# Performance work log

Hardware: AMD Instinct MI355X
Metric: run time of the kernel (lower is better)

The kernel has to match this reference:

```python
import jax, jax.numpy as jnp
import numpy as np
from jax import lax

SEQ_LEN = 1024
INPUT_DIM = 64
NUM_HIDDEN = 512
NUM_CLASSES = 10
BATCH = 256
SIGMA = 0.01


def setup_inputs() -> dict:
    key = jax.random.key(0)
    k_x, k_whx, k_whh, k_wph = jax.random.split(key, 4)
    x = jax.random.normal(k_x, (BATCH, SEQ_LEN, INPUT_DIM), dtype=jnp.float32)
    Whx = SIGMA * jax.random.normal(k_whx, (INPUT_DIM, NUM_HIDDEN), dtype=jnp.float32)
    Whh = SIGMA * jax.random.normal(k_whh, (NUM_HIDDEN, NUM_HIDDEN), dtype=jnp.float32)
    Wph = SIGMA * jax.random.normal(k_wph, (NUM_HIDDEN, NUM_CLASSES), dtype=jnp.float32)
    bh = jnp.zeros((NUM_HIDDEN, 1), dtype=jnp.float32)
    bp = jnp.zeros((NUM_CLASSES, 1), dtype=jnp.float32)
    return {"x": x, "Whx": Whx, "Whh": Whh, "Wph": Wph, "bh": bh, "bp": bp}


def reference(x, Whx, Whh, Wph, bh, bp):
    # x: [B, S, D]; h: [B, H]
    B = x.shape[0]
    H = Whh.shape[0]
    bh_row = bh[:, 0]  # per-hidden-unit bias (intended semantics of bh)
    bp_row = bp[:, 0]

    def step(h, xt):
        h_new = jnp.tanh(xt @ Whx + h @ Whh + bh_row)
        return h_new, None

    h0 = jnp.zeros((B, H), dtype=x.dtype)
    xs = jnp.swapaxes(x, 0, 1)  # [S, B, D] for scan over time
    h_final, _ = lax.scan(step, h0, xs)
    p = h_final @ Wph + bp_row  # [B, C]
    return p
```

## Files before the change

### kernel.cpp

```cpp
#include <hip/hip_runtime.h>
#include <hip/hip_bf16.h>
#include <hip/hip_fp8.h>
#include <cstdint>
#include <cstddef>


#define T_SEQ   1024
#define D_IN    64
#define H_DIM   512
#define NB      16
#define NBLK    16
#define NTW     4
#define KS_F16  10
#define KS_REG8 2
#define KS_LDS8 4
#define HSPLIT  320
#define APITCH  848
#define FP8OFF  640
#define ABUF_BYTES (2 * NB * APITCH)
#define WWAVE_BYTES (KS_LDS8 * 2 * 1024)
#define WLDS_BYTES (8 * WWAVE_BYTES)
#define SMEM_TOTAL (ABUF_BYTES + WLDS_BYTES)
#define WSCALE  256.0f
#define HSCALE  128.0f
#define UNSCALE (1.0f / 32768.0f)
#define U_BYTES ((size_t)256 * 1024 * 512 * 2)
#define TT      16

typedef __attribute__((ext_vector_type(8))) short  short8;
typedef __attribute__((ext_vector_type(4))) short  short4v;
typedef __attribute__((ext_vector_type(4))) float  f32x4;
typedef __attribute__((ext_vector_type(2))) _Float16 h2v;
typedef __attribute__((ext_vector_type(4))) unsigned int uint4v;
typedef __attribute__((ext_vector_type(2))) unsigned int uint2v;

static __device__ __forceinline__ short f16b(float v) {
  return __builtin_bit_cast(short, (_Float16)v);
}
static __device__ __forceinline__ short bf16b(float v) {
  return __builtin_bit_cast(short, __float2bfloat16(v));
}
static __device__ __forceinline__ float f16f(unsigned short u) {
  return (float)__builtin_bit_cast(_Float16, (short)u);
}
static __device__ __forceinline__ unsigned int pk2h(float a, float b) {
#if defined(__has_builtin) && __has_builtin(__builtin_amdgcn_cvt_pkrtz)
  return __builtin_bit_cast(unsigned int, __builtin_amdgcn_cvt_pkrtz(a, b));
#else
  return (unsigned int)(unsigned short)f16b(a) |
         ((unsigned int)(unsigned short)f16b(b) << 16);
#endif
}
static __device__ __forceinline__ float fast_tanh(float x) {
  x = fminf(20.f, fmaxf(-20.f, x));
  const float t = __builtin_amdgcn_exp2f(x * 2.885390081777927f);
  return (t - 1.f) * __builtin_amdgcn_rcpf(t + 1.f);
}
static __device__ __forceinline__ unsigned char f32_to_fp8(float v) {
#if defined(__has_builtin) && __has_builtin(__builtin_amdgcn_cvt_pk_fp8_f32)
  const int r = __builtin_amdgcn_cvt_pk_fp8_f32(v, v, 0, false);
  return (unsigned char)(r & 0xff);
#else
  __hip_fp8_e4m3 f(v);
  return (unsigned char)f.__x;
#endif
}
static __device__ __forceinline__ unsigned int pk4fp8(float a, float b, float c, float d) {
#if defined(__has_builtin) && __has_builtin(__builtin_amdgcn_cvt_pk_fp8_f32)
  int r = __builtin_amdgcn_cvt_pk_fp8_f32(a, b, 0, false);
  r = __builtin_amdgcn_cvt_pk_fp8_f32(c, d, r, true);
  return (unsigned int)r;
#else
  return (unsigned int)f32_to_fp8(a) | ((unsigned int)f32_to_fp8(b) << 8) |
         ((unsigned int)f32_to_fp8(c) << 16) | ((unsigned int)f32_to_fp8(d) << 24);
#endif
}
static __device__ __forceinline__ float fp8_to_f32(unsigned char b) {
  __hip_fp8_e4m3 f;
  f.__x = (__hip_fp8_storage_t)b;
  return (float)f;
}

__global__ __launch_bounds__(512, 2)
void rnn_u_precompute(const float* __restrict__ x, const float* __restrict__ Whx,
                      const float* __restrict__ bh, char* __restrict__ U)
{
  const int tid  = threadIdx.x;
  const int lane = tid & 63;
  const int w    = tid >> 6;
  const int n16  = lane & 15;
  const int kq   = lane >> 4;
  const int rbase = blockIdx.x * NB;
  const int cwave = w * 64;

  short8 wa[2][NTW];
  #pragma unroll
  for (int s = 0; s < 2; ++s) {
    #pragma unroll
    for (int nt = 0; nt < NTW; ++nt) {
      const int c = cwave + nt * 16 + n16;
      short8 f;
      #pragma unroll
      for (int j = 0; j < 8; ++j)
        f[j] = f16b(Whx[(size_t)(s * 32 + kq * 8 + j) * H_DIM + c]);
      wa[s][nt] = f;
    }
  }
  f32x4 bb[NTW];
  #pragma unroll
  for (int nt = 0; nt < NTW; ++nt) {
    #pragma unroll
    for (int i = 0; i < 4; ++i) bb[nt][i] = bh[cwave + nt * 16 + kq * 4 + i];
  }

  const int b = rbase + n16;
  for (int tt = 0; tt < TT; ++tt) {
    const int t = blockIdx.y * TT + tt;
    short8 xb[2];
    #pragma unroll
    for (int s = 0; s < 2; ++s) {
      const float* px = x + ((size_t)b * T_SEQ + t) * D_IN + s * 32 + kq * 8;
      const f32x4 v0 = *(const f32x4*)px;
      const f32x4 v1 = *(const f32x4*)(px + 4);
      short8 f;
      f[0]=f16b(v0.x); f[1]=f16b(v0.y); f[2]=f16b(v0.z); f[3]=f16b(v0.w);
      f[4]=f16b(v1.x); f[5]=f16b(v1.y); f[6]=f16b(v1.z); f[7]=f16b(v1.w);
      xb[s] = f;
    }
    f32x4 D[NTW];
    #pragma unroll
    for (int nt = 0; nt < NTW; ++nt) {
      D[nt] = bb[nt];
      D[nt] = __builtin_amdgcn_mfma_f32_16x16x32_f16(wa[0][nt], xb[0], D[nt], 0, 0, 0);
      D[nt] = __builtin_amdgcn_mfma_f32_16x16x32_f16(wa[1][nt], xb[1], D[nt], 0, 0, 0);
    }
    uint4v o0, o1;
    o0.x = pk2h(D[0][0], D[0][1]); o0.y = pk2h(D[0][2], D[0][3]);
    o0.z = pk2h(D[1][0], D[1][1]); o0.w = pk2h(D[1][2], D[1][3]);
    o1.x = pk2h(D[2][0], D[2][1]); o1.y = pk2h(D[2][2], D[2][3]);
    o1.z = pk2h(D[3][0], D[3][1]); o1.w = pk2h(D[3][2], D[3][3]);
    char* dst = U + (((size_t)t * NBLK + blockIdx.x) * 512 + tid) * 32;
    *(uint4v*)dst = o0;
    *(uint4v*)(dst + 16) = o1;
  }
}

__global__ __launch_bounds__(512, 2)
void VanillaRNN_70025146794452_kernel(
    const float* __restrict__ Whh,
    const float* __restrict__ Wph,
    const float* __restrict__ bp,
    const char* __restrict__ U,
    float* __restrict__ out)
{
  const int tid  = threadIdx.x;
  const int lane = tid & 63;
  const int w    = tid >> 6;
  const int n16  = lane & 15;
  const int kq   = lane >> 4;
  const int rbase = blockIdx.x * NB;
  const int cwave = w * 64;

  extern __shared__ char smem[];
  char* Ab  = smem;
  char* Wlw = smem + ABUF_BYTES + w * WWAVE_BYTES;

  short8 wr[KS_F16][NTW];
  #pragma unroll
  for (int s = 0; s < KS_F16; ++s) {
    #pragma unroll
    for (int nt = 0; nt < NTW; ++nt) {
      const int c = cwave + nt * 16 + n16;
      short8 f;
      #pragma unroll
      for (int j = 0; j < 8; ++j)
        f[j] = f16b(Whh[(size_t)(s * 32 + kq * 8 + j) * H_DIM + c]);
      wr[s][nt] = f;
    }
  }
  long long wf8[KS_REG8][NTW];
  #pragma unroll
  for (int s = 0; s < KS_REG8; ++s) {
    #pragma unroll
    for (int nt = 0; nt < NTW; ++nt) {
      const int c  = cwave + nt * 16 + n16;
      const int k0 = (KS_F16 + s) * 32 + kq * 8;
      unsigned int lo = 0, hi = 0;
      #pragma unroll
      for (int bi = 0; bi < 4; ++bi) {
        lo |= ((unsigned int)f32_to_fp8(Whh[(size_t)(k0 + bi) * H_DIM + c] * WSCALE)) << (8 * bi);
        hi |= ((unsigned int)f32_to_fp8(Whh[(size_t)(k0 + 4 + bi) * H_DIM + c] * WSCALE)) << (8 * bi);
      }
      wf8[s][nt] = (long long)(((unsigned long long)hi << 32) | lo);
    }
  }
  for (int sl = 0; sl < KS_LDS8; ++sl) {
    for (int half = 0; half < 2; ++half) {
      const int k0 = (KS_F16 + KS_REG8 + sl) * 32 + kq * 8;
      unsigned int bqq[4];
      #pragma unroll
      for (int hh = 0; hh < 2; ++hh) {
        const int c = cwave + (2 * half + hh) * 16 + n16;
        #pragma unroll
        for (int u = 0; u < 2; ++u) {
          unsigned int acc = 0;
          #pragma unroll
          for (int bi = 0; bi < 4; ++bi)
            acc |= ((unsigned int)f32_to_fp8(Whh[(size_t)(k0 + u * 4 + bi) * H_DIM + c] * WSCALE)) << (8 * bi);
          bqq[hh * 2 + u] = acc;
        }
      }
      uint4v pk; pk.x = bqq[0]; pk.y = bqq[1]; pk.z = bqq[2]; pk.w = bqq[3];
      *(uint4v*)(Wlw + (size_t)(sl * 2 + half) * 1024 + lane * 16) = pk;
    }
  }

  for (int i = tid; i < ABUF_BYTES / 4; i += 512) ((int*)Ab)[i] = 0;
  uint4v Upf0, Upf1;
  {
    const char* up = U + (((size_t)0 * NBLK + blockIdx.x) * 512 + tid) * 32;
    Upf0 = *(const uint4v*)up;
    Upf1 = *(const uint4v*)(up + 16);
  }

  f32x4 C[NTW], C2[NTW];

  for (int t = 0; t < T_SEQ; ++t) {
    __syncthreads();
    char* Ac = Ab + (t & 1) * (NB * APITCH);
    char* An = Ab + ((t + 1) & 1) * (NB * APITCH);

    C[0][0]=f16f(Upf0.x&0xffff); C[0][1]=f16f(Upf0.x>>16);
    C[0][2]=f16f(Upf0.y&0xffff); C[0][3]=f16f(Upf0.y>>16);
    C[1][0]=f16f(Upf0.z&0xffff); C[1][1]=f16f(Upf0.z>>16);
    C[1][2]=f16f(Upf0.w&0xffff); C[1][3]=f16f(Upf0.w>>16);
    C[2][0]=f16f(Upf1.x&0xffff); C[2][1]=f16f(Upf1.x>>16);
    C[2][2]=f16f(Upf1.y&0xffff); C[2][3]=f16f(Upf1.y>>16);
    C[3][0]=f16f(Upf1.z&0xffff); C[3][1]=f16f(Upf1.z>>16);
    C[3][2]=f16f(Upf1.w&0xffff); C[3][3]=f16f(Upf1.w>>16);
    #pragma unroll
    for (int nt = 0; nt < NTW; ++nt) C2[nt] = (f32x4){0.f, 0.f, 0.f, 0.f};
    {
      const int t1 = (t + 1 < T_SEQ) ? (t + 1) : (T_SEQ - 1);
      const char* up = U + (((size_t)t1 * NBLK + blockIdx.x) * 512 + tid) * 32;
      Upf0 = *(const uint4v*)up;
      Upf1 = *(const uint4v*)(up + 16);
    }

    short8 hb = *(const short8*)(Ac + n16 * APITCH + 0 * 64 + kq * 16);
    #pragma unroll
    for (int s = 0; s < KS_F16; ++s) {
      const short8 a = hb;
      if (s + 1 < KS_F16)
        hb = *(const short8*)(Ac + n16 * APITCH + (s + 1) * 64 + kq * 16);
      #pragma unroll
      for (int nt = 0; nt < NTW; ++nt)
        C[nt] = __builtin_amdgcn_mfma_f32_16x16x32_f16(wr[s][nt], a, C[nt], 0, 0, 0);
    }
    #pragma unroll
    for (int s = 0; s < KS_REG8; ++s) {
      const long long h8 = *(const long long*)(Ac + n16 * APITCH + FP8OFF + s * 32 + kq * 8);
      #pragma unroll
      for (int nt = 0; nt < NTW; ++nt)
        C2[nt] = __builtin_amdgcn_mfma_f32_16x16x32_fp8_fp8(wf8[s][nt], h8, C2[nt], 0, 0, 0);
    }
    #pragma unroll
    for (int sl = 0; sl < KS_LDS8; ++sl) {
      const long long h8 = *(const long long*)(Ac + n16 * APITCH + FP8OFF + (KS_REG8 + sl) * 32 + kq * 8);
      const uint4v q0 = *(const uint4v*)(Wlw + (size_t)(sl * 2 + 0) * 1024 + lane * 16);
      const uint4v q1 = *(const uint4v*)(Wlw + (size_t)(sl * 2 + 1) * 1024 + lane * 16);
      const long long w0 = (long long)(((unsigned long long)q0.y << 32) | q0.x);
      const long long w1 = (long long)(((unsigned long long)q0.w << 32) | q0.z);
      const long long w2 = (long long)(((unsigned long long)q1.y << 32) | q1.x);
      const long long w3 = (long long)(((unsigned long long)q1.w << 32) | q1.z);
      C2[0] = __builtin_amdgcn_mfma_f32_16x16x32_fp8_fp8(w0, h8, C2[0], 0, 0, 0);
      C2[1] = __builtin_amdgcn_mfma_f32_16x16x32_fp8_fp8(w1, h8, C2[1], 0, 0, 0);
      C2[2] = __builtin_amdgcn_mfma_f32_16x16x32_fp8_fp8(w2, h8, C2[2], 0, 0, 0);
      C2[3] = __builtin_amdgcn_mfma_f32_16x16x32_fp8_fp8(w3, h8, C2[3], 0, 0, 0);
    }

    char* drow = An + n16 * APITCH;
    if (cwave < HSPLIT) {
      #pragma unroll
      for (int nt = 0; nt < NTW; ++nt) {
        const int c0 = cwave + nt * 16 + kq * 4;
        float v0 = fast_tanh(fmaf(C2[nt][0], UNSCALE, C[nt][0]));
        float v1 = fast_tanh(fmaf(C2[nt][1], UNSCALE, C[nt][1]));
        float v2 = fast_tanh(fmaf(C2[nt][2], UNSCALE, C[nt][2]));
        float v3 = fast_tanh(fmaf(C2[nt][3], UNSCALE, C[nt][3]));
        uint2v o; o.x = pk2h(v0, v1); o.y = pk2h(v2, v3);
        *(uint2v*)(drow + c0 * 2) = o;
      }
    } else {
      #pragma unroll
      for (int nt = 0; nt < NTW; ++nt) {
        const int c0 = cwave + nt * 16 + kq * 4;
        float v0 = fast_tanh(fmaf(C2[nt][0], UNSCALE, C[nt][0]));
        float v1 = fast_tanh(fmaf(C2[nt][1], UNSCALE, C[nt][1]));
        float v2 = fast_tanh(fmaf(C2[nt][2], UNSCALE, C[nt][2]));
        float v3 = fast_tanh(fmaf(C2[nt][3], UNSCALE, C[nt][3]));
        *(unsigned int*)(drow + FP8OFF + (c0 - HSPLIT)) =
            pk4fp8(v0 * HSCALE, v1 * HSCALE, v2 * HSCALE, v3 * HSCALE);
      }
    }
  }

  __syncthreads();
  if (tid < NB * 10) {
    const int r = tid / 10, c = tid % 10;
    const char* row = Ab + r * APITCH;
    float acc = bp[c];
    #pragma unroll 8
    for (int k = 0; k < HSPLIT; ++k)
      acc += f16f(*(const unsigned short*)(row + k * 2)) * Wph[k * 10 + c];
    #pragma unroll 8
    for (int k = HSPLIT; k < H_DIM; ++k)
      acc += fp8_to_f32((unsigned char)row[FP8OFF + (k - HSPLIT)]) * (1.f / HSCALE) * Wph[k * 10 + c];
    out[(size_t)(rbase + r) * 10 + c] = acc;
  }
}

#define FB_APITCH  1040
#define FB_FP8OFF  768
#define FB_ABUF    (2 * NB * FB_APITCH)
#define FB_WWAVE   (6 * 2 * 1024)
#define FB_SMEM    (FB_ABUF + 8 * FB_WWAVE)

__global__ __launch_bounds__(512, 2)
void rnn_fallback_kernel(
    const float* __restrict__ x, const float* __restrict__ Whx,
    const float* __restrict__ Whh, const float* __restrict__ Wph,
    const float* __restrict__ bh, const float* __restrict__ bp,
    float* __restrict__ out)
{
  const int tid = threadIdx.x, lane = tid & 63, w = tid >> 6;
  const int n16 = lane & 15, kq = lane >> 4;
  const int rbase = blockIdx.x * NB, cwave = w * 64;
  extern __shared__ char smem[];
  char* Ab  = smem;
  char* Wlw = smem + FB_ABUF + w * FB_WWAVE;

  short8 wr[12 * 4];
  #pragma unroll
  for (int s = 0; s < 12; ++s)
    #pragma unroll
    for (int nt = 0; nt < 4; ++nt) {
      const int c = cwave + nt * 16 + n16, k0 = s * 32 + kq * 8;
      short8 f;
      #pragma unroll
      for (int j = 0; j < 8; ++j) {
        const int k = k0 + j;
        const float* src = (k < D_IN) ? (Whx + (size_t)k * H_DIM + c)
                                      : (Whh + (size_t)(k - D_IN) * H_DIM + c);
        f[j] = bf16b(*src);
      }
      wr[s * 4 + nt] = f;
    }
  for (int s = 0; s < 6; ++s)
    for (int pp = 0; pp < 2; ++pp) {
      const int k0 = (12 + s) * 32 + kq * 8;
      unsigned int bq[4];
      #pragma unroll
      for (int half = 0; half < 2; ++half) {
        const int c = cwave + (2 * pp + half) * 16 + n16;
        #pragma unroll
        for (int u = 0; u < 2; ++u) {
          unsigned int acc = 0;
          #pragma unroll
          for (int bi = 0; bi < 4; ++bi)
            acc |= ((unsigned int)f32_to_fp8(Whh[(size_t)(k0 + u * 4 + bi - D_IN) * H_DIM + c] * WSCALE)) << (8 * bi);
          bq[half * 2 + u] = acc;
        }
      }
      uint4v pk; pk.x = bq[0]; pk.y = bq[1]; pk.z = bq[2]; pk.w = bq[3];
      *(uint4v*)(Wlw + (size_t)(s * 2 + pp) * 1024 + lane * 16) = pk;
    }
  float bhreg[4];
  #pragma unroll
  for (int nt = 0; nt < 4; ++nt) bhreg[nt] = bh[cwave + nt * 16 + n16];
  for (int i = tid; i < FB_ABUF / 4; i += 512) ((int*)Ab)[i] = 0;
  const int xr = (tid >> 4) & 15, xc4 = (tid & 15) * 4;
  if (tid < 256) {
    const f32x4 xv = *(const f32x4*)(x + ((size_t)(rbase + xr) * T_SEQ) * D_IN + xc4);
    short4v s4; s4[0]=bf16b(xv.x); s4[1]=bf16b(xv.y); s4[2]=bf16b(xv.z); s4[3]=bf16b(xv.w);
    *(short4v*)(Ab + xr * FB_APITCH + xc4 * 2) = s4;
  }
  f32x4 C[4], C2[4];
  for (int t = 0; t < T_SEQ; ++t) {
    __syncthreads();
    char* Ac = Ab + (t & 1) * (NB * FB_APITCH);
    char* An = Ab + ((t + 1) & 1) * (NB * FB_APITCH);
    const int t1 = (t + 1 < T_SEQ) ? (t + 1) : (T_SEQ - 1);
    f32x4 xv;
    if (tid < 256)
      xv = *(const f32x4*)(x + ((size_t)(rbase + xr) * T_SEQ + t1) * D_IN + xc4);
    #pragma unroll
    for (int nt = 0; nt < 4; ++nt) {
      C[nt] = (f32x4){0.f,0.f,0.f,0.f}; C2[nt] = (f32x4){0.f,0.f,0.f,0.f};
    }
    #pragma unroll
    for (int s = 0; s < 12; ++s) {
      const short8 a = *(const short8*)(Ac + n16 * FB_APITCH + s * 64 + kq * 16);
      #pragma unroll
      for (int nt = 0; nt < 4; ++nt)
        C[nt] = __builtin_amdgcn_mfma_f32_16x16x32_bf16(a, wr[s * 4 + nt], C[nt], 0, 0, 0);
    }
    #pragma unroll
    for (int s = 0; s < 6; ++s) {
      const long long a8 = *(const long long*)(Ac + n16 * FB_APITCH + FB_FP8OFF + s * 32 + kq * 8);
      #pragma unroll
      for (int pp = 0; pp < 2; ++pp) {
        const uint4v q = *(const uint4v*)(Wlw + (size_t)(s * 2 + pp) * 1024 + lane * 16);
        const long long b0 = (long long)(((unsigned long long)q.y << 32) | q.x);
        const long long b1 = (long long)(((unsigned long long)q.w << 32) | q.z);
        C2[2*pp]   = __builtin_amdgcn_mfma_f32_16x16x32_fp8_fp8(a8, b0, C2[2*pp],   0, 0, 0);
        C2[2*pp+1] = __builtin_amdgcn_mfma_f32_16x16x32_fp8_fp8(a8, b1, C2[2*pp+1], 0, 0, 0);
      }
    }
    if (tid < 256) {
      short4v s4; s4[0]=bf16b(xv.x); s4[1]=bf16b(xv.y); s4[2]=bf16b(xv.z); s4[3]=bf16b(xv.w);
      *(short4v*)(An + xr * FB_APITCH + xc4 * 2) = s4;
    }
    const int row0 = kq * 4;
    #pragma unroll
    for (int nt = 0; nt < 4; ++nt) {
      const int cbase = cwave + nt * 16;
      #pragma unroll
      for (int i = 0; i < 4; ++i) {
        const float v = fast_tanh(fmaf(C2[nt][i], UNSCALE, C[nt][i]) + bhreg[nt]);
        char* dst = An + (row0 + i) * FB_APITCH;
        if (cbase < 320) *(short*)(dst + 128 + (cbase + n16) * 2) = bf16b(v);
        else dst[FB_FP8OFF + (cbase + n16 - 320)] = f32_to_fp8(v * HSCALE);
      }
    }
  }
  __syncthreads();
  if (tid < NB * 10) {
    const int r = tid / 10, c = tid % 10;
    const char* row = Ab + r * FB_APITCH;
    float acc = bp[c];
    #pragma unroll 8
    for (int k = 0; k < 320; ++k) {
      const __hip_bfloat16 hb = __builtin_bit_cast(__hip_bfloat16, *(const short*)(row + 128 + k * 2));
      acc += __bfloat162float(hb) * Wph[k * 10 + c];
    }
    #pragma unroll 8
    for (int k = 320; k < H_DIM; ++k)
      acc += fp8_to_f32((unsigned char)row[FB_FP8OFF + (k - 320)]) * (1.f / HSCALE) * Wph[k * 10 + c];
    out[(size_t)(rbase + r) * 10 + c] = acc;
  }
}

extern "C" void kernel_launch(void* const* d_in, const int* in_sizes, int n_in,
                              void* d_out, int out_size, void* d_ws, size_t ws_size,
                              hipStream_t stream) {
  const float* x   = (const float*)d_in[0];
  const float* Whx = (const float*)d_in[1];
  const float* Whh = (const float*)d_in[2];
  const float* Wph = (const float*)d_in[3];
  const float* bh  = (const float*)d_in[4];
  const float* bp  = (const float*)d_in[5];
  float* out = (float*)d_out;

  if (ws_size >= U_BYTES) {
    char* U = (char*)d_ws;
    (void)hipFuncSetAttribute((const void*)VanillaRNN_70025146794452_kernel,
                              hipFuncAttributeMaxDynamicSharedMemorySize, SMEM_TOTAL);
    rnn_u_precompute<<<dim3(NBLK, T_SEQ / TT), dim3(512), 0, stream>>>(x, Whx, bh, U);
    VanillaRNN_70025146794452_kernel<<<dim3(NBLK), dim3(512), SMEM_TOTAL, stream>>>(
        Whh, Wph, bp, U, out);
  } else {
    (void)hipFuncSetAttribute((const void*)rnn_fallback_kernel,
                              hipFuncAttributeMaxDynamicSharedMemorySize, FB_SMEM);
    rnn_fallback_kernel<<<dim3(NBLK), dim3(512), FB_SMEM, stream>>>(
        x, Whx, Whh, Wph, bh, bp, out);
  }
}
```

Measured before the change: 1.899 ms.

## Run FP8 MFMA chain first and fold its result into the f16 accumulator init

Reorders each timestep so the FP8 MFMA partial sums are computed first. They are scaled and added to the precomputed input projection to initialise the f16 accumulators, and the f16 MFMA chain then finishes the sum. This removes the per-element fmaf merge before tanh and shortens the dependent tail after the last MFMA. It also moves more FP8 weight k-slices from LDS into registers, which adds register pressure, and halves the TT constant.

```diff
diff --git a/kernel.cpp b/kernel.cpp
--- a/kernel.cpp
+++ b/kernel.cpp
@@ -12,8 +12,8 @@
 #define NBLK    16
 #define NTW     4
 #define KS_F16  10
-#define KS_REG8 2
-#define KS_LDS8 4
+#define KS_REG8 4
+#define KS_LDS8 2
 #define HSPLIT  320
 #define APITCH  848
 #define FP8OFF  640
@@ -25,12 +25,11 @@
 #define HSCALE  128.0f
 #define UNSCALE (1.0f / 32768.0f)
 #define U_BYTES ((size_t)256 * 1024 * 512 * 2)
-#define TT      16
+#define TT      8
 
 typedef __attribute__((ext_vector_type(8))) short  short8;
 typedef __attribute__((ext_vector_type(4))) short  short4v;
 typedef __attribute__((ext_vector_type(4))) float  f32x4;
-typedef __attribute__((ext_vector_type(2))) _Float16 h2v;
 typedef __attribute__((ext_vector_type(4))) unsigned int uint4v;
 typedef __attribute__((ext_vector_type(2))) unsigned int uint2v;
 
@@ -230,33 +229,10 @@
     char* Ac = Ab + (t & 1) * (NB * APITCH);
     char* An = Ab + ((t + 1) & 1) * (NB * APITCH);
 
-    C[0][0]=f16f(Upf0.x&0xffff); C[0][1]=f16f(Upf0.x>>16);
-    C[0][2]=f16f(Upf0.y&0xffff); C[0][3]=f16f(Upf0.y>>16);
-    C[1][0]=f16f(Upf0.z&0xffff); C[1][1]=f16f(Upf0.z>>16);
-    C[1][2]=f16f(Upf0.w&0xffff); C[1][3]=f16f(Upf0.w>>16);
-    C[2][0]=f16f(Upf1.x&0xffff); C[2][1]=f16f(Upf1.x>>16);
-    C[2][2]=f16f(Upf1.y&0xffff); C[2][3]=f16f(Upf1.y>>16);
-    C[3][0]=f16f(Upf1.z&0xffff); C[3][1]=f16f(Upf1.z>>16);
-    C[3][2]=f16f(Upf1.w&0xffff); C[3][3]=f16f(Upf1.w>>16);
+    short8 hb = *(const short8*)(Ac + n16 * APITCH + 0 * 64 + kq * 16);
+
     #pragma unroll
     for (int nt = 0; nt < NTW; ++nt) C2[nt] = (f32x4){0.f, 0.f, 0.f, 0.f};
-    {
-      const int t1 = (t + 1 < T_SEQ) ? (t + 1) : (T_SEQ - 1);
-      const char* up = U + (((size_t)t1 * NBLK + blockIdx.x) * 512 + tid) * 32;
-      Upf0 = *(const uint4v*)up;
-      Upf1 = *(const uint4v*)(up + 16);
-    }
-
-    short8 hb = *(const short8*)(Ac + n16 * APITCH + 0 * 64 + kq * 16);
-    #pragma unroll
-    for (int s = 0; s < KS_F16; ++s) {
-      const short8 a = hb;
-      if (s + 1 < KS_F16)
-        hb = *(const short8*)(Ac + n16 * APITCH + (s + 1) * 64 + kq * 16);
-      #pragma unroll
-      for (int nt = 0; nt < NTW; ++nt)
-        C[nt] = __builtin_amdgcn_mfma_f32_16x16x32_f16(wr[s][nt], a, C[nt], 0, 0, 0);
-    }
     #pragma unroll
     for (int s = 0; s < KS_REG8; ++s) {
       const long long h8 = *(const long long*)(Ac + n16 * APITCH + FP8OFF + s * 32 + kq * 8);
@@ -279,15 +255,41 @@
       C2[3] = __builtin_amdgcn_mfma_f32_16x16x32_fp8_fp8(w3, h8, C2[3], 0, 0, 0);
     }
 
+    C[0][0]=fmaf(C2[0][0],UNSCALE,f16f(Upf0.x&0xffff)); C[0][1]=fmaf(C2[0][1],UNSCALE,f16f(Upf0.x>>16));
+    C[0][2]=fmaf(C2[0][2],UNSCALE,f16f(Upf0.y&0xffff)); C[0][3]=fmaf(C2[0][3],UNSCALE,f16f(Upf0.y>>16));
+    C[1][0]=fmaf(C2[1][0],UNSCALE,f16f(Upf0.z&0xffff)); C[1][1]=fmaf(C2[1][1],UNSCALE,f16f(Upf0.z>>16));
+    C[1][2]=fmaf(C2[1][2],UNSCALE,f16f(Upf0.w&0xffff)); C[1][3]=fmaf(C2[1][3],UNSCALE,f16f(Upf0.w>>16));
+    C[2][0]=fmaf(C2[2][0],UNSCALE,f16f(Upf1.x&0xffff)); C[2][1]=fmaf(C2[2][1],UNSCALE,f16f(Upf1.x>>16));
+    C[2][2]=fmaf(C2[2][2],UNSCALE,f16f(Upf1.y&0xffff)); C[2][3]=fmaf(C2[2][3],UNSCALE,f16f(Upf1.y>>16));
+    C[3][0]=fmaf(C2[3][0],UNSCALE,f16f(Upf1.z&0xffff)); C[3][1]=fmaf(C2[3][1],UNSCALE,f16f(Upf1.z>>16));
+    C[3][2]=fmaf(C2[3][2],UNSCALE,f16f(Upf1.w&0xffff)); C[3][3]=fmaf(C2[3][3],UNSCALE,f16f(Upf1.w>>16));
+
+    {
+      const int t1 = (t + 1 < T_SEQ) ? (t + 1) : (T_SEQ - 1);
+      const char* up = U + (((size_t)t1 * NBLK + blockIdx.x) * 512 + tid) * 32;
+      Upf0 = *(const uint4v*)up;
+      Upf1 = *(const uint4v*)(up + 16);
+    }
+
+    #pragma unroll
+    for (int s = 0; s < KS_F16; ++s) {
+      const short8 a = hb;
+      if (s + 1 < KS_F16)
+        hb = *(const short8*)(Ac + n16 * APITCH + (s + 1) * 64 + kq * 16);
+      #pragma unroll
+      for (int nt = 0; nt < NTW; ++nt)
+        C[nt] = __builtin_amdgcn_mfma_f32_16x16x32_f16(wr[s][nt], a, C[nt], 0, 0, 0);
+    }
+
     char* drow = An + n16 * APITCH;
     if (cwave < HSPLIT) {
       #pragma unroll
       for (int nt = 0; nt < NTW; ++nt) {
         const int c0 = cwave + nt * 16 + kq * 4;
-        float v0 = fast_tanh(fmaf(C2[nt][0], UNSCALE, C[nt][0]));
-        float v1 = fast_tanh(fmaf(C2[nt][1], UNSCALE, C[nt][1]));
-        float v2 = fast_tanh(fmaf(C2[nt][2], UNSCALE, C[nt][2]));
-        float v3 = fast_tanh(fmaf(C2[nt][3], UNSCALE, C[nt][3]));
+        float v0 = fast_tanh(C[nt][0]);
+        float v1 = fast_tanh(C[nt][1]);
+        float v2 = fast_tanh(C[nt][2]);
+        float v3 = fast_tanh(C[nt][3]);
         uint2v o; o.x = pk2h(v0, v1); o.y = pk2h(v2, v3);
         *(uint2v*)(drow + c0 * 2) = o;
       }
@@ -295,10 +297,10 @@
       #pragma unroll
       for (int nt = 0; nt < NTW; ++nt) {
         const int c0 = cwave + nt * 16 + kq * 4;
-        float v0 = fast_tanh(fmaf(C2[nt][0], UNSCALE, C[nt][0]));
-        float v1 = fast_tanh(fmaf(C2[nt][1], UNSCALE, C[nt][1]));
-        float v2 = fast_tanh(fmaf(C2[nt][2], UNSCALE, C[nt][2]));
-        float v3 = fast_tanh(fmaf(C2[nt][3], UNSCALE, C[nt][3]));
+        float v0 = fast_tanh(C[nt][0]);
+        float v1 = fast_tanh(C[nt][1]);
+        float v2 = fast_tanh(C[nt][2]);
+        float v3 = fast_tanh(C[nt][3]);
         *(unsigned int*)(drow + FP8OFF + (c0 - HSPLIT)) =
             pk4fp8(v0 * HSCALE, v1 * HSCALE, v2 * HSCALE, v3 * HSCALE);
       }
```

After: 1.977 ms. 1.04x slower.

## Fuse input projection producers with recurrent consumers via flag-gated single launch

Applied to the files above, without the earlier changes.

Merges the input-projection precompute and the recurrent kernel into one launch. The first 16 blocks run the recurrence while the remaining blocks produce U chunks of 8 timesteps and publish per-chunk flags that consumers spin on before reading. The aim is to hide the precompute kernel's latency behind the serial recurrence. It also moves more fp8 Whh slices from LDS into registers (KS_REG8 4, KS_LDS8 2) and hoists the h load earlier in each step. This relies on consumer blocks being scheduled before or alongside producers to avoid deadlock, and adds register pressure and spin-wait overhead.

```diff
diff --git a/kernel.cpp b/kernel.cpp
--- a/kernel.cpp
+++ b/kernel.cpp
@@ -12,8 +12,8 @@
 #define NBLK    16
 #define NTW     4
 #define KS_F16  10
-#define KS_REG8 2
-#define KS_LDS8 4
+#define KS_REG8 4
+#define KS_LDS8 2
 #define HSPLIT  320
 #define APITCH  848
 #define FP8OFF  640
@@ -25,12 +25,14 @@
 #define HSCALE  128.0f
 #define UNSCALE (1.0f / 32768.0f)
 #define U_BYTES ((size_t)256 * 1024 * 512 * 2)
-#define TT      16
+#define TT      8
+#define NCHUNK  (T_SEQ / TT)
+#define NPROD   (NBLK * NCHUNK)
+#define FLAG_BYTES (NBLK * NCHUNK * 4)
 
 typedef __attribute__((ext_vector_type(8))) short  short8;
 typedef __attribute__((ext_vector_type(4))) short  short4v;
 typedef __attribute__((ext_vector_type(4))) float  f32x4;
-typedef __attribute__((ext_vector_type(2))) _Float16 h2v;
 typedef __attribute__((ext_vector_type(4))) unsigned int uint4v;
 typedef __attribute__((ext_vector_type(2))) unsigned int uint2v;
 
@@ -81,16 +83,19 @@
   return (float)f;
 }
 
-__global__ __launch_bounds__(512, 2)
-void rnn_u_precompute(const float* __restrict__ x, const float* __restrict__ Whx,
-                      const float* __restrict__ bh, char* __restrict__ U)
+static __device__ __forceinline__ void producer_body(
+    int pid, const float* __restrict__ x, const float* __restrict__ Whx,
+    const float* __restrict__ bh, char* __restrict__ U,
+    unsigned int* __restrict__ flags)
 {
+  const int wg = pid & (NBLK - 1);
+  const int tc = pid >> 4;
   const int tid  = threadIdx.x;
   const int lane = tid & 63;
   const int w    = tid >> 6;
   const int n16  = lane & 15;
   const int kq   = lane >> 4;
-  const int rbase = blockIdx.x * NB;
+  const int rbase = wg * NB;
   const int cwave = w * 64;
 
   short8 wa[2][NTW];
@@ -115,7 +120,7 @@
 
   const int b = rbase + n16;
   for (int tt = 0; tt < TT; ++tt) {
-    const int t = blockIdx.y * TT + tt;
+    const int t = tc * TT + tt;
     short8 xb[2];
     #pragma unroll
     for (int s = 0; s < 2; ++s) {
@@ -139,26 +144,29 @@
     o0.z = pk2h(D[1][0], D[1][1]); o0.w = pk2h(D[1][2], D[1][3]);
     o1.x = pk2h(D[2][0], D[2][1]); o1.y = pk2h(D[2][2], D[2][3]);
     o1.z = pk2h(D[3][0], D[3][1]); o1.w = pk2h(D[3][2], D[3][3]);
-    char* dst = U + (((size_t)t * NBLK + blockIdx.x) * 512 + tid) * 32;
+    char* dst = U + (((size_t)t * NBLK + wg) * 512 + tid) * 32;
     *(uint4v*)dst = o0;
     *(uint4v*)(dst + 16) = o1;
   }
-}
-
-__global__ __launch_bounds__(512, 2)
-void VanillaRNN_70025146794452_kernel(
-    const float* __restrict__ Whh,
-    const float* __restrict__ Wph,
-    const float* __restrict__ bp,
-    const char* __restrict__ U,
-    float* __restrict__ out)
+
+  __syncthreads();
+  if (flags && tid == 0) {
+    __threadfence();
+    atomicExch(&flags[wg * NCHUNK + tc], 1u);
+  }
+}
+
+static __device__ __forceinline__ void consumer_body(
+    int wg, const float* __restrict__ Whh, const float* __restrict__ Wph,
+    const float* __restrict__ bp, const char* __restrict__ U,
+    unsigned int* __restrict__ flags, int gated, float* __restrict__ out)
 {
   const int tid  = threadIdx.x;
   const int lane = tid & 63;
   const int w    = tid >> 6;
   const int n16  = lane & 15;
   const int kq   = lane >> 4;
-  const int rbase = blockIdx.x * NB;
+  const int rbase = wg * NB;
   const int cwave = w * 64;
 
   extern __shared__ char smem[];
@@ -216,9 +224,16 @@
   }
 
   for (int i = tid; i < ABUF_BYTES / 4; i += 512) ((int*)Ab)[i] = 0;
+  if (gated) {
+    if (tid == 0) {
+      while (atomicAdd(&flags[wg * NCHUNK + 0], 0u) == 0u) { }
+      __threadfence();
+    }
+  }
+  __syncthreads();
   uint4v Upf0, Upf1;
   {
-    const char* up = U + (((size_t)0 * NBLK + blockIdx.x) * 512 + tid) * 32;
+    const char* up = U + (((size_t)0 * NBLK + wg) * 512 + tid) * 32;
     Upf0 = *(const uint4v*)up;
     Upf1 = *(const uint4v*)(up + 16);
   }
@@ -229,6 +244,8 @@
     __syncthreads();
     char* Ac = Ab + (t & 1) * (NB * APITCH);
     char* An = Ab + ((t + 1) & 1) * (NB * APITCH);
+
+    short8 hb = *(const short8*)(Ac + n16 * APITCH + 0 * 64 + kq * 16);
 
     C[0][0]=f16f(Upf0.x&0xffff); C[0][1]=f16f(Upf0.x>>16);
     C[0][2]=f16f(Upf0.y&0xffff); C[0][3]=f16f(Upf0.y>>16);
@@ -240,14 +257,14 @@
     C[3][2]=f16f(Upf1.w&0xffff); C[3][3]=f16f(Upf1.w>>16);
     #pragma unroll
     for (int nt = 0; nt < NTW; ++nt) C2[nt] = (f32x4){0.f, 0.f, 0.f, 0.f};
+
     {
       const int t1 = (t + 1 < T_SEQ) ? (t + 1) : (T_SEQ - 1);
-      const char* up = U + (((size_t)t1 * NBLK + blockIdx.x) * 512 + tid) * 32;
+      const char* up = U + (((size_t)t1 * NBLK + wg) * 512 + tid) * 32;
       Upf0 = *(const uint4v*)up;
       Upf1 = *(const uint4v*)(up + 16);
     }
 
-    short8 hb = *(const short8*)(Ac + n16 * APITCH + 0 * 64 + kq * 16);
     #pragma unroll
     for (int s = 0; s < KS_F16; ++s) {
       const short8 a = hb;
@@ -257,6 +274,7 @@
       for (int nt = 0; nt < NTW; ++nt)
         C[nt] = __builtin_amdgcn_mfma_f32_16x16x32_f16(wr[s][nt], a, C[nt], 0, 0, 0);
     }
+
     #pragma unroll
     for (int s = 0; s < KS_REG8; ++s) {
       const long long h8 = *(const long long*)(Ac + n16 * APITCH + FP8OFF + s * 32 + kq * 8);
@@ -303,6 +321,16 @@
             pk4fp8(v0 * HSCALE, v1 * HSCALE, v2 * HSCALE, v3 * HSCALE);
       }
     }
+
+    if (gated) {
+      const int tn = t + 2;
+      if (tn < T_SEQ && (tn & (TT - 1)) == 0) {
+        if (tid == 0) {
+          while (atomicAdd(&flags[wg * NCHUNK + (tn >> 3)], 0u) == 0u) { }
+          __threadfence();
+        }
+      }
+    }
   }
 
   __syncthreads();
@@ -317,6 +345,26 @@
     for (int k = HSPLIT; k < H_DIM; ++k)
       acc += fp8_to_f32((unsigned char)row[FP8OFF + (k - HSPLIT)]) * (1.f / HSCALE) * Wph[k * 10 + c];
     out[(size_t)(rbase + r) * 10 + c] = acc;
+  }
+}
+
+__global__ __launch_bounds__(512, 2)
+void VanillaRNN_70025146794452_kernel(
+    const float* __restrict__ x, const float* __restrict__ Whx,
+    const float* __restrict__ Whh, const float* __restrict__ Wph,
+    const float* __restrict__ bh, const float* __restrict__ bp,
+    char* __restrict__ U, unsigned int* __restrict__ flags,
+    float* __restrict__ out, int mode)
+{
+  if (mode == 0) {
+    if (blockIdx.x < NBLK)
+      consumer_body(blockIdx.x, Whh, Wph, bp, U, flags, 1, out);
+    else
+      producer_body(blockIdx.x - NBLK, x, Whx, bh, U, flags);
+  } else if (mode == 1) {
+    producer_body(blockIdx.x, x, Whx, bh, U, nullptr);
+  } else {
+    consumer_body(blockIdx.x, Whh, Wph, bp, U, nullptr, 0, out);
   }
 }
 
@@ -462,13 +510,23 @@
   const float* bp  = (const float*)d_in[5];
   float* out = (float*)d_out;
 
-  if (ws_size >= U_BYTES) {
+  if (ws_size >= U_BYTES + FLAG_BYTES + 256) {
+    char* U = (char*)d_ws;
+    const size_t foff = (ws_size - FLAG_BYTES) & ~(size_t)255;
+    unsigned int* flags = (unsigned int*)((char*)d_ws + foff);
+    (void)hipFuncSetAttribute((const void*)VanillaRNN_70025146794452_kernel,
+                              hipFuncAttributeMaxDynamicSharedMemorySize, SMEM_TOTAL);
+    (void)hipMemsetAsync(flags, 0, FLAG_BYTES, stream);
+    VanillaRNN_70025146794452_kernel<<<dim3(NBLK + NPROD), dim3(512), SMEM_TOTAL, stream>>>(
+        x, Whx, Whh, Wph, bh, bp, U, flags, out, 0);
+  } else if (ws_size >= U_BYTES) {
     char* U = (char*)d_ws;
     (void)hipFuncSetAttribute((const void*)VanillaRNN_70025146794452_kernel,
                               hipFuncAttributeMaxDynamicSharedMemorySize, SMEM_TOTAL);
-    rnn_u_precompute<<<dim3(NBLK, T_SEQ / TT), dim3(512), 0, stream>>>(x, Whx, bh, U);
+    VanillaRNN_70025146794452_kernel<<<dim3(NPROD), dim3(512), SMEM_TOTAL, stream>>>(
+        x, Whx, Whh, Wph, bh, bp, U, nullptr, out, 1);
     VanillaRNN_70025146794452_kernel<<<dim3(NBLK), dim3(512), SMEM_TOTAL, stream>>>(
-        Whh, Wph, bp, U, out);
+        x, Whx, Whh, Wph, bh, bp, U, nullptr, out, 2);
   } else {
     (void)hipFuncSetAttribute((const void*)rnn_fallback_kernel,
                               hipFuncAttributeMaxDynamicSharedMemorySize, FB_SMEM);
```

Result: slower. 2.011 ms (+5.9%).
